# Kernel tuning notes

Hardware: AMD Instinct MI355X
Metric: run time of the kernel (lower is better)

The kernel has to match this reference:

```python
import jax, jax.numpy as jnp
import numpy as np

NUM_HEADS = 16
HEAD_DIM = 64
MODEL_DIM = NUM_HEADS * HEAD_DIM  # 1024
N_TOKENS = 121
BATCH = 1024
DISTURB_HEADS = np.array([0, 3], dtype=int)


def setup_inputs() -> dict:
    key = jax.random.key(0)
    ks = jax.random.split(key, 8)
    scale = 1.0 / np.sqrt(MODEL_DIM)
    return {
        "query": jax.random.normal(ks[0], (BATCH, MODEL_DIM), dtype=jnp.float32),
        "key": jax.random.normal(ks[1], (BATCH, N_TOKENS, MODEL_DIM), dtype=jnp.float32),
        "value": jax.random.normal(ks[2], (BATCH, N_TOKENS, MODEL_DIM), dtype=jnp.float32),
        "Wq": jax.random.normal(ks[3], (MODEL_DIM, MODEL_DIM), dtype=jnp.float32) * scale,
        "bq": jnp.zeros((MODEL_DIM,), dtype=jnp.float32),
        "Wk": jax.random.normal(ks[4], (MODEL_DIM, MODEL_DIM), dtype=jnp.float32) * scale,
        "bk": jnp.zeros((MODEL_DIM,), dtype=jnp.float32),
        "Wv": jax.random.normal(ks[5], (MODEL_DIM, MODEL_DIM), dtype=jnp.float32) * scale,
        "bv": jnp.zeros((MODEL_DIM,), dtype=jnp.float32),
    }


def reference(query, key, value, Wq, bq, Wk, bk, Wv, bv):
    B, N, _ = key.shape
    H, d = NUM_HEADS, HEAD_DIM
    # Linear projections (plain GEMMs)
    q_proj = query @ Wq + bq            # [B, H*d]
    k_proj = key @ Wk + bk              # [B, N, H*d]
    v_proj = value @ Wv + bv            # [B, N, H*d]

    q = q_proj.reshape(B, H, d)         # [B, H, d]
    k = k_proj.reshape(B, N, H, d)      # [B, N, H, d]
    v = v_proj.reshape(B, N, H, d)

    # single-query scores per head: [B, H, N]
    scores = jnp.einsum('bhd,bnhd->bhn', q, k)
    # head-wise disturb override: masked heads get all-ones scores
    mask = jnp.zeros((H,), dtype=bool).at[DISTURB_HEADS].set(True)[None, :, None]
    scores = jnp.where(mask, jnp.ones_like(scores), scores)
    # note: original scales by sqrt(d * H), not sqrt(d)
    scores = scores / jnp.sqrt(jnp.asarray(d * H, dtype=scores.dtype))
    weights = jax.nn.softmax(scores, axis=-1)   # [B, H, N]
    output = jnp.einsum('bhn,bnhd->bhd', weights, v).reshape(B, H * d)
    return (output, weights)
```

## Files before the change

### kernel.cpp

```cpp
#include <hip/hip_runtime.h>
#include <hip/hip_bf16.h>

#define NHEADS 16
#define HDIM   64
#define MDIM   1024
#define NTOK   121
#define NBATCH 1024

typedef __attribute__((ext_vector_type(4))) float f32x4;
typedef __attribute__((ext_vector_type(4))) short s16x4;
typedef __attribute__((ext_vector_type(8))) short s16x8;

#define WAIT_VM(n)  asm volatile("s_waitcnt vmcnt(" #n ")" ::: "memory")
#define WAIT_LGKM0() asm volatile("s_waitcnt lgkmcnt(0)" ::: "memory")

__device__ __forceinline__ short f2bf(float f) {
  __hip_bfloat16 h = __float2bfloat16(f);
  return __builtin_bit_cast(short, h);
}

#define GLDS(gptr, lptr)                                                        \
  __builtin_amdgcn_global_load_lds(                                             \
      (const __attribute__((address_space(1))) void*)(gptr),                    \
      (__attribute__((address_space(3))) void*)(lptr), 16, 0, 0)

__global__ __launch_bounds__(256) void kTransW(const float* __restrict__ Wq,
                                               const float* __restrict__ Wk,
                                               const float* __restrict__ Wv,
                                               short* __restrict__ Wt) {
  int bid = blockIdx.x;
  int m = bid >> 8, tile = bid & 255;
  int tr = tile >> 4, tc = tile & 15;
  const float* W = (m == 0) ? Wq : (m == 1) ? Wk : Wv;
  short* T = Wt + (size_t)m * (MDIM * MDIM);
  __shared__ float tl[64][68];
  int t = threadIdx.x;
  int c4 = t & 15, r0 = t >> 4;
#pragma unroll
  for (int i = 0; i < 4; ++i) {
    int kr = r0 + i * 16;
    f32x4 v = *(const f32x4*)(W + (size_t)(tr * 64 + kr) * MDIM + tc * 64 + c4 * 4);
    *(f32x4*)&tl[kr][c4 * 4] = v;
  }
  __syncthreads();
#pragma unroll
  for (int i = 0; i < 4; ++i) {
    int n = r0 + i * 16;
    s16x4 o;
    o.x = f2bf(tl[c4 * 4 + 0][n]);
    o.y = f2bf(tl[c4 * 4 + 1][n]);
    o.z = f2bf(tl[c4 * 4 + 2][n]);
    o.w = f2bf(tl[c4 * 4 + 3][n]);
    *(s16x4*)(T + (size_t)(tc * 64 + n) * MDIM + tr * 64 + c4 * 4) = o;
  }
}

__device__ __forceinline__ void gemm_core(const float* __restrict__ A, int mrows,
                                          const short* __restrict__ Wt, int c0,
                                          short* Alds, short* Bl0, short* Bl1,
                                          f32x4 acc[4][4], int t) {
  int wid = t >> 6, lane = t & 63;
  int wr = wid >> 1, wc = wid & 1;
  int li = lane & 15, lg = lane >> 4;
  int kq = t & 15, r0s = t >> 4;
#pragma unroll
  for (int fm = 0; fm < 4; ++fm)
#pragma unroll
    for (int fn = 0; fn < 4; ++fn) acc[fm][fn] = (f32x4)0.0f;

  int rhi[4];
#pragma unroll
  for (int i = 0; i < 4; ++i) {
    int row = r0s + 64 + (i << 4);
    rhi[i] = row < mrows ? row : mrows - 1;
  }
#pragma unroll
  for (int i = 0; i < 4; ++i) {
    int cl = wid * 32 + i * 8 + (lane >> 3);
    int jg = (lane & 7) ^ (cl & 7);
    GLDS(Wt + (size_t)(c0 + cl) * MDIM + jg * 8, Bl0 + (wid * 32 + i * 8) * 64);
  }
  f32x4 rLo[4];
#pragma unroll
  for (int i = 0; i < 4; ++i)
    rLo[i] = *(const f32x4*)(A + (size_t)(r0s + (i << 4)) * MDIM + kq * 4);

  for (int kt = 0; kt < 16; ++kt) {
    int k0 = kt * 64;
    short* Bcur = (kt & 1) ? Bl1 : Bl0;
    short* Bnxt = (kt & 1) ? Bl0 : Bl1;
    int kn = (kt < 15) ? k0 + 64 : 0;

    f32x4 rHi[4];
#pragma unroll
    for (int i = 0; i < 4; ++i)
      rHi[i] = *(const f32x4*)(A + (size_t)rhi[i] * MDIM + k0 + kq * 4);

    WAIT_VM(4);
    __builtin_amdgcn_s_barrier();
#pragma unroll
    for (int i = 0; i < 4; ++i) {
      int row = r0s + (i << 4);
      s16x4 b4;
      b4.x = f2bf(rLo[i].x); b4.y = f2bf(rLo[i].y);
      b4.z = f2bf(rLo[i].z); b4.w = f2bf(rLo[i].w);
      int byte = (row * 128 + kq * 8) ^ ((row & 7) << 4);
      *(s16x4*)((char*)Alds + byte) = b4;
    }
#pragma unroll
    for (int i = 0; i < 4; ++i) {
      int cl = wid * 32 + i * 8 + (lane >> 3);
      int jg = (lane & 7) ^ (cl & 7);
      GLDS(Wt + (size_t)(c0 + cl) * MDIM + kn + jg * 8, Bnxt + (wid * 32 + i * 8) * 64);
    }
    WAIT_VM(4);
#pragma unroll
    for (int i = 0; i < 4; ++i) {
      int row = r0s + 64 + (i << 4);
      s16x4 b4;
      b4.x = f2bf(rHi[i].x); b4.y = f2bf(rHi[i].y);
      b4.z = f2bf(rHi[i].z); b4.w = f2bf(rHi[i].w);
      int byte = (row * 128 + kq * 8) ^ ((row & 7) << 4);
      *(s16x4*)((char*)Alds + byte) = b4;
    }
#pragma unroll
    for (int i = 0; i < 4; ++i)
      rLo[i] = *(const f32x4*)(A + (size_t)(r0s + (i << 4)) * MDIM + kn + kq * 4);

    WAIT_LGKM0();
    __builtin_amdgcn_s_barrier();
#pragma unroll
    for (int ks = 0; ks < 2; ++ks) {
      s16x8 af[4];
      int kb = ks * 64 + lg * 16;
#pragma unroll
      for (int fm = 0; fm < 4; ++fm) {
        int row = wr * 64 + fm * 16 + li;
        int byte = (row * 128 + kb) ^ ((row & 7) << 4);
        af[fm] = *(s16x8*)((char*)Alds + byte);
      }
#pragma unroll
      for (int fn = 0; fn < 4; ++fn) {
        int col = wc * 64 + fn * 16 + li;
        int byte = (col * 128 + kb) ^ ((col & 7) << 4);
        s16x8 bfv = *(s16x8*)((char*)Bcur + byte);
#pragma unroll
        for (int fm = 0; fm < 4; ++fm)
          acc[fm][fn] = __builtin_amdgcn_mfma_f32_16x16x32_bf16(af[fm], bfv,
                                                                acc[fm][fn], 0, 0, 0);
      }
    }
  }
}

__global__ __launch_bounds__(256, 3) void kQProj(const float* __restrict__ query,
                                                 const short* __restrict__ WtQ,
                                                 const float* __restrict__ bq,
                                                 float* __restrict__ qp) {
  __shared__ alignas(16) short Alds[128 * 64];
  __shared__ alignas(16) short Bl0[128 * 64];
  __shared__ alignas(16) short Bl1[128 * 64];
  int bid = blockIdx.x;
  int rt = bid >> 3, ct = bid & 7;
  f32x4 acc[4][4];
  int t = threadIdx.x;
  gemm_core(query + (size_t)rt * 128 * MDIM, 128, WtQ, ct * 128, Alds, Bl0, Bl1, acc, t);
  int wid = t >> 6, lane = t & 63;
  int wr = wid >> 1, wc = wid & 1, li = lane & 15, lg = lane >> 4;
#pragma unroll
  for (int fn = 0; fn < 4; ++fn) {
    int col = ct * 128 + wc * 64 + fn * 16 + li;
    float bqv = bq[col];
#pragma unroll
    for (int fm = 0; fm < 4; ++fm)
#pragma unroll
      for (int rr = 0; rr < 4; ++rr) {
        int row = rt * 128 + wr * 64 + fm * 16 + lg * 4 + rr;
        qp[(size_t)row * MDIM + col] = acc[fm][fn][rr] + bqv;
      }
  }
}

__global__ __launch_bounds__(256, 3) void kG(const float* __restrict__ qp,
                                             const short* __restrict__ WtK,
                                             short* __restrict__ g) {
  __shared__ alignas(16) short Alds[128 * 64];
  __shared__ alignas(16) short Blds[128 * 64];
  int bid = blockIdx.x;
  int h = bid >> 6, bt = (bid >> 3) & 7, it = bid & 7;
  int t = threadIdx.x;
  int wid = t >> 6, lane = t & 63;
  int wr = wid >> 1, wc = wid & 1, li = lane & 15, lg = lane >> 4;
  int kq = t & 15, r0s = t >> 4;
#pragma unroll
  for (int i = 0; i < 8; ++i) {
    int r = r0s + 16 * i;
    f32x4 v = *(const f32x4*)(qp + (size_t)(bt * 128 + r) * MDIM + h * 64 + kq * 4);
    s16x4 b4;
    b4.x = f2bf(v.x); b4.y = f2bf(v.y); b4.z = f2bf(v.z); b4.w = f2bf(v.w);
    int byte = (r * 128 + kq * 8) ^ ((r & 7) << 4);
    *(s16x4*)((char*)Alds + byte) = b4;
  }
  {
    int jr = t >> 2, qc = t & 3;
#pragma unroll
    for (int q = 0; q < 4; ++q) {
      s16x8 v = *(const s16x8*)(WtK + (size_t)(h * 64 + jr) * MDIM + it * 128 +
                                qc * 32 + q * 8);
#pragma unroll
      for (int e = 0; e < 8; ++e) {
        int i = qc * 32 + q * 8 + e;
        int byte = (i * 128 + jr * 2) ^ ((i & 7) << 4);
        *(short*)((char*)Blds + byte) = v[e];
      }
    }
  }
  __syncthreads();
  f32x4 acc[4][4];
#pragma unroll
  for (int fm = 0; fm < 4; ++fm)
#pragma unroll
    for (int fn = 0; fn < 4; ++fn) acc[fm][fn] = (f32x4)0.0f;
#pragma unroll
  for (int ks = 0; ks < 2; ++ks) {
    int kb = ks * 64 + lg * 16;
    s16x8 af[4];
#pragma unroll
    for (int fm = 0; fm < 4; ++fm) {
      int row = wr * 64 + fm * 16 + li;
      int byte = (row * 128 + kb) ^ ((row & 7) << 4);
      af[fm] = *(s16x8*)((char*)Alds + byte);
    }
#pragma unroll
    for (int fn = 0; fn < 4; ++fn) {
      int col = wc * 64 + fn * 16 + li;
      int byte = (col * 128 + kb) ^ ((col & 7) << 4);
      s16x8 bfv = *(s16x8*)((char*)Blds + byte);
#pragma unroll
      for (int fm = 0; fm < 4; ++fm)
        acc[fm][fn] = __builtin_amdgcn_mfma_f32_16x16x32_bf16(af[fm], bfv,
                                                              acc[fm][fn], 0, 0, 0);
    }
  }
#pragma unroll
  for (int fm = 0; fm < 4; ++fm)
#pragma unroll
    for (int rr = 0; rr < 4; ++rr) {
      int b = bt * 128 + wr * 64 + fm * 16 + lg * 4 + rr;
      short* gp = g + ((size_t)b * 16 + h) * 1024 + it * 128;
#pragma unroll
      for (int fn = 0; fn < 4; ++fn)
        gp[wc * 64 + fn * 16 + li] = f2bf(acc[fm][fn][rr]);
    }
}

__global__ __launch_bounds__(512, 4) void kW(const float* __restrict__ key,
                                             const short* __restrict__ g,
                                             float* __restrict__ weights) {
  __shared__ alignas(16) short Klds[128 * 64];
  __shared__ alignas(16) short Glds[16 * 1024];
  __shared__ float s_lds[16][132];
  int b = blockIdx.x;
  int t = threadIdx.x;
  int wid = t >> 6, lane = t & 63, li = lane & 15, lg = lane >> 4;
  int kq = t & 15, r0s = t >> 4;
  int rcl[4];
#pragma unroll
  for (int i = 0; i < 4; ++i) {
    int r = r0s + 32 * i;
    rcl[i] = r < NTOK ? r : NTOK - 1;
  }
  const float* A = key + (size_t)b * NTOK * MDIM;
  const short* gb = g + (size_t)b * 16384;
#pragma unroll
  for (int q = 0; q < 4; ++q) {
    int c = q * 512 + t;
    s16x8 v = *(const s16x8*)(gb + c * 8);
    int byte = ((c >> 7) * 2048 + (c & 127) * 16) ^ (((c >> 7) & 7) << 4);
    *(s16x8*)((char*)Glds + byte) = v;
  }
  f32x4 rA[4];
#pragma unroll
  for (int i = 0; i < 4; ++i)
    rA[i] = *(const f32x4*)(A + (size_t)rcl[i] * MDIM + kq * 4);
  f32x4 acc = (f32x4)0.0f;

  for (int kt = 0; kt < 16; ++kt) {
    int kn = (kt < 15) ? (kt + 1) * 64 : 0;
    WAIT_VM(0);
    __builtin_amdgcn_s_barrier();
#pragma unroll
    for (int i = 0; i < 4; ++i) {
      int row = r0s + 32 * i;
      s16x4 b4;
      b4.x = f2bf(rA[i].x); b4.y = f2bf(rA[i].y);
      b4.z = f2bf(rA[i].z); b4.w = f2bf(rA[i].w);
      int byte = (row * 128 + kq * 8) ^ ((row & 7) << 4);
      *(s16x4*)((char*)Klds + byte) = b4;
    }
#pragma unroll
    for (int i = 0; i < 4; ++i)
      rA[i] = *(const f32x4*)(A + (size_t)rcl[i] * MDIM + kn + kq * 4);
    WAIT_LGKM0();
    __builtin_amdgcn_s_barrier();
#pragma unroll
    for (int ks = 0; ks < 2; ++ks) {
      int kb = ks * 64 + lg * 16;
      int row = wid * 16 + li;
      s16x8 af = *(s16x8*)((char*)Klds + ((row * 128 + kb) ^ ((row & 7) << 4)));
      int kel = kt * 64 + ks * 32 + lg * 8;
      s16x8 bf = *(s16x8*)((char*)Glds + ((li * 2048 + kel * 2) ^ ((li & 7) << 4)));
      acc = __builtin_amdgcn_mfma_f32_16x16x32_bf16(af, bf, acc, 0, 0, 0);
    }
  }
#pragma unroll
  for (int rr = 0; rr < 4; ++rr) s_lds[li][wid * 16 + lg * 4 + rr] = acc[rr];
  __syncthreads();
#pragma unroll
  for (int hh = 0; hh < 2; ++hh) {
    int h = wid * 2 + hh;
    int n0 = lane, n1 = lane + 64;
    bool v0 = (n0 < NTOK), v1 = (n1 < NTOK);
    float w0, w1;
    if (h == 0 || h == 3) {
      w0 = 1.f / NTOK; w1 = 1.f / NTOK;
    } else {
      const float kinv = 1.f / 32.f;
      float s0 = v0 ? s_lds[h][n0] * kinv : -1e30f;
      float s1 = v1 ? s_lds[h][n1] * kinv : -1e30f;
      float m = fmaxf(s0, s1);
#pragma unroll
      for (int msk = 1; msk < 64; msk <<= 1) m = fmaxf(m, __shfl_xor(m, msk));
      float e0 = v0 ? __expf(s0 - m) : 0.f;
      float e1 = v1 ? __expf(s1 - m) : 0.f;
      float s = e0 + e1;
#pragma unroll
      for (int msk = 1; msk < 64; msk <<= 1) s += __shfl_xor(s, msk);
      float inv = 1.f / s;
      w0 = e0 * inv; w1 = e1 * inv;
    }
    float* wp = weights + ((size_t)b * NHEADS + h) * NTOK;
    if (v0) wp[n0] = w0;
    if (v1) wp[n1] = w1;
  }
}

__global__ __launch_bounds__(512, 4) void kV(const float* __restrict__ value,
                                             const float* __restrict__ weights,
                                             float* __restrict__ vbar) {
  __shared__ float w_lds[16][128];
  int b = blockIdx.x;
  int t = threadIdx.x;
  int grp = t >> 7, ic = t & 127;
#pragma unroll
  for (int q = 0; q < 4; ++q) {
    int idx = q * 512 + t;
    int h = idx >> 7, n = idx & 127;
    w_lds[h][n] = (n < NTOK) ? weights[((size_t)b * NHEADS + h) * NTOK + n] : 0.f;
  }
  __syncthreads();
  const float* V = value + (size_t)b * NTOK * MDIM;
  f32x4 a0[4], a1[4];
#pragma unroll
  for (int hh = 0; hh < 4; ++hh) { a0[hh] = (f32x4)0.0f; a1[hh] = (f32x4)0.0f; }
#pragma unroll 2
  for (int n = 0; n < NTOK; ++n) {
    f32x4 v0 = *(const f32x4*)(V + (size_t)n * MDIM + ic * 8);
    f32x4 v1 = *(const f32x4*)(V + (size_t)n * MDIM + ic * 8 + 4);
#pragma unroll
    for (int hh = 0; hh < 4; ++hh) {
      float wn = w_lds[grp * 4 + hh][n];
      a0[hh] += wn * v0;
      a1[hh] += wn * v1;
    }
  }
#pragma unroll
  for (int hh = 0; hh < 4; ++hh) {
    float* vp = vbar + ((size_t)b * 16 + grp * 4 + hh) * 1024 + ic * 8;
    *(f32x4*)vp = a0[hh];
    *(f32x4*)(vp + 4) = a1[hh];
  }
}

__global__ __launch_bounds__(256, 3) void kO(const float* __restrict__ vbar,
                                             const short* __restrict__ WtV,
                                             const float* __restrict__ bv,
                                             float* __restrict__ outp) {
  __shared__ alignas(16) short Alds[128 * 64];
  __shared__ alignas(16) short Blds[64 * 64];
  int bid = blockIdx.x;
  int bt = bid >> 4, h = bid & 15;
  int t = threadIdx.x;
  int wid = t >> 6, lane = t & 63;
  int wr = wid >> 1, wc = wid & 1, li = lane & 15, lg = lane >> 4;
  int kq = t & 15, r0s = t >> 4;
  const float* A = vbar + (size_t)bt * 128 * 16384 + (size_t)h * 1024;
  f32x4 acc[4][2];
#pragma unroll
  for (int fm = 0; fm < 4; ++fm)
#pragma unroll
    for (int fn = 0; fn < 2; ++fn) acc[fm][fn] = (f32x4)0.0f;
  f32x4 rLo[4];
#pragma unroll
  for (int i = 0; i < 4; ++i)
    rLo[i] = *(const f32x4*)(A + (size_t)(r0s + 16 * i) * 16384 + kq * 4);

  for (int kt = 0; kt < 16; ++kt) {
    int k0 = kt * 64;
    __syncthreads();
    f32x4 rHi[4];
#pragma unroll
    for (int i = 0; i < 4; ++i)
      rHi[i] = *(const f32x4*)(A + (size_t)(r0s + 64 + 16 * i) * 16384 + k0 + kq * 4);
#pragma unroll
    for (int j = 0; j < 2; ++j) {
      int cl = wid * 16 + j * 8 + (lane >> 3);
      int jg = (lane & 7) ^ (cl & 7);
      GLDS(WtV + (size_t)(h * 64 + cl) * MDIM + k0 + jg * 8,
           Blds + (wid * 16 + j * 8) * 64);
    }
#pragma unroll
    for (int i = 0; i < 4; ++i) {
      int row = r0s + 16 * i;
      s16x4 b4;
      b4.x = f2bf(rLo[i].x); b4.y = f2bf(rLo[i].y);
      b4.z = f2bf(rLo[i].z); b4.w = f2bf(rLo[i].w);
      int byte = (row * 128 + kq * 8) ^ ((row & 7) << 4);
      *(s16x4*)((char*)Alds + byte) = b4;
    }
#pragma unroll
    for (int i = 0; i < 4; ++i) {
      int row = r0s + 64 + 16 * i;
      s16x4 b4;
      b4.x = f2bf(rHi[i].x); b4.y = f2bf(rHi[i].y);
      b4.z = f2bf(rHi[i].z); b4.w = f2bf(rHi[i].w);
      int byte = (row * 128 + kq * 8) ^ ((row & 7) << 4);
      *(s16x4*)((char*)Alds + byte) = b4;
    }
    __syncthreads();
    {
      int k1 = (kt < 15) ? k0 + 64 : 0;
#pragma unroll
      for (int i = 0; i < 4; ++i)
        rLo[i] = *(const f32x4*)(A + (size_t)(r0s + 16 * i) * 16384 + k1 + kq * 4);
    }
#pragma unroll
    for (int ks = 0; ks < 2; ++ks) {
      int kb = ks * 64 + lg * 16;
      s16x8 af[4];
#pragma unroll
      for (int fm = 0; fm < 4; ++fm) {
        int row = wr * 64 + fm * 16 + li;
        int byte = (row * 128 + kb) ^ ((row & 7) << 4);
        af[fm] = *(s16x8*)((char*)Alds + byte);
      }
#pragma unroll
      for (int fn = 0; fn < 2; ++fn) {
        int col = wc * 32 + fn * 16 + li;
        int byte = (col * 128 + kb) ^ ((col & 7) << 4);
        s16x8 bfv = *(s16x8*)((char*)Blds + byte);
#pragma unroll
        for (int fm = 0; fm < 4; ++fm)
          acc[fm][fn] = __builtin_amdgcn_mfma_f32_16x16x32_bf16(af[fm], bfv,
                                                                acc[fm][fn], 0, 0, 0);
      }
    }
  }
#pragma unroll
  for (int fn = 0; fn < 2; ++fn) {
    int cg = h * 64 + wc * 32 + fn * 16 + li;
    float bvv = bv[cg];
#pragma unroll
    for (int fm = 0; fm < 4; ++fm)
#pragma unroll
      for (int rr = 0; rr < 4; ++rr) {
        int row = bt * 128 + wr * 64 + fm * 16 + lg * 4 + rr;
        outp[(size_t)row * MDIM + cg] = acc[fm][fn][rr] + bvv;
      }
  }
}

extern "C" void kernel_launch(void* const* d_in, const int* in_sizes, int n_in,
                              void* d_out, int out_size, void* d_ws, size_t ws_size,
                              hipStream_t stream) {
  const float* query = (const float*)d_in[0];
  const float* key   = (const float*)d_in[1];
  const float* value = (const float*)d_in[2];
  const float* Wq    = (const float*)d_in[3];
  const float* bq    = (const float*)d_in[4];
  const float* Wk    = (const float*)d_in[5];
  const float* bk    = (const float*)d_in[6];
  const float* Wv    = (const float*)d_in[7];
  const float* bv    = (const float*)d_in[8];
  (void)bk;

  float* out     = (float*)d_out;
  float* weights = out + (size_t)NBATCH * MDIM;

  char* ws = (char*)d_ws;
  short* Wt   = (short*)ws;
  float* qp   = (float*)(ws + 6u  * 1024 * 1024);
  short* g    = (short*)(ws + 10u * 1024 * 1024);
  float* vbar = (float*)(ws + 48u * 1024 * 1024);

  kTransW<<<dim3(768),  dim3(256), 0, stream>>>(Wq, Wk, Wv, Wt);
  kQProj <<<dim3(64),   dim3(256), 0, stream>>>(query, Wt, bq, qp);
  kG     <<<dim3(1024), dim3(256), 0, stream>>>(qp, Wt + (size_t)MDIM * MDIM, g);
  kW     <<<dim3(1024), dim3(512), 0, stream>>>(key, g, weights);
  kV     <<<dim3(1024), dim3(512), 0, stream>>>(value, weights, vbar);
  kO     <<<dim3(128),  dim3(256), 0, stream>>>(vbar, Wt + 2 * (size_t)MDIM * MDIM,
                                                bv, out);
}
```

Before: 379.2 us.

## Double-buffer key tiles in kW and store vbar as bf16 for direct LDS loads

After: 315.0 us. 16.9% less time.

```diff
diff --git a/kernel.cpp b/kernel.cpp
--- a/kernel.cpp
+++ b/kernel.cpp
@@ -254,10 +254,11 @@
     }
 }
 
-__global__ __launch_bounds__(512, 4) void kW(const float* __restrict__ key,
-                                             const short* __restrict__ g,
-                                             float* __restrict__ weights) {
-  __shared__ alignas(16) short Klds[128 * 64];
+__global__ __launch_bounds__(512) void kW(const float* __restrict__ key,
+                                          const short* __restrict__ g,
+                                          float* __restrict__ weights) {
+  __shared__ alignas(16) short Kl0[128 * 64];
+  __shared__ alignas(16) short Kl1[128 * 64];
   __shared__ alignas(16) short Glds[16 * 1024];
   __shared__ float s_lds[16][132];
   int b = blockIdx.x;
@@ -279,36 +280,69 @@
     int byte = ((c >> 7) * 2048 + (c & 127) * 16) ^ (((c >> 7) & 7) << 4);
     *(s16x8*)((char*)Glds + byte) = v;
   }
-  f32x4 rA[4];
+  f32x4 rA0[4], rA1[4];
 #pragma unroll
   for (int i = 0; i < 4; ++i)
-    rA[i] = *(const f32x4*)(A + (size_t)rcl[i] * MDIM + kq * 4);
+    rA0[i] = *(const f32x4*)(A + (size_t)rcl[i] * MDIM + kq * 4);
+#pragma unroll
+  for (int i = 0; i < 4; ++i)
+    rA1[i] = *(const f32x4*)(A + (size_t)rcl[i] * MDIM + 64 + kq * 4);
+  WAIT_LGKM0();
+  __builtin_amdgcn_s_barrier();
   f32x4 acc = (f32x4)0.0f;
 
-  for (int kt = 0; kt < 16; ++kt) {
-    int kn = (kt < 15) ? (kt + 1) * 64 : 0;
-    WAIT_VM(0);
-    __builtin_amdgcn_s_barrier();
+  for (int kt = 0; kt < 16; kt += 2) {
+    WAIT_VM(4);
 #pragma unroll
     for (int i = 0; i < 4; ++i) {
       int row = r0s + 32 * i;
       s16x4 b4;
-      b4.x = f2bf(rA[i].x); b4.y = f2bf(rA[i].y);
-      b4.z = f2bf(rA[i].z); b4.w = f2bf(rA[i].w);
+      b4.x = f2bf(rA0[i].x); b4.y = f2bf(rA0[i].y);
+      b4.z = f2bf(rA0[i].z); b4.w = f2bf(rA0[i].w);
       int byte = (row * 128 + kq * 8) ^ ((row & 7) << 4);
-      *(s16x4*)((char*)Klds + byte) = b4;
-    }
-#pragma unroll
-    for (int i = 0; i < 4; ++i)
-      rA[i] = *(const f32x4*)(A + (size_t)rcl[i] * MDIM + kn + kq * 4);
+      *(s16x4*)((char*)Kl0 + byte) = b4;
+    }
+    {
+      int kn = (kt + 2 < 16) ? (kt + 2) * 64 : 0;
+#pragma unroll
+      for (int i = 0; i < 4; ++i)
+        rA0[i] = *(const f32x4*)(A + (size_t)rcl[i] * MDIM + kn + kq * 4);
+    }
     WAIT_LGKM0();
     __builtin_amdgcn_s_barrier();
 #pragma unroll
     for (int ks = 0; ks < 2; ++ks) {
       int kb = ks * 64 + lg * 16;
       int row = wid * 16 + li;
-      s16x8 af = *(s16x8*)((char*)Klds + ((row * 128 + kb) ^ ((row & 7) << 4)));
+      s16x8 af = *(s16x8*)((char*)Kl0 + ((row * 128 + kb) ^ ((row & 7) << 4)));
       int kel = kt * 64 + ks * 32 + lg * 8;
+      s16x8 bf = *(s16x8*)((char*)Glds + ((li * 2048 + kel * 2) ^ ((li & 7) << 4)));
+      acc = __builtin_amdgcn_mfma_f32_16x16x32_bf16(af, bf, acc, 0, 0, 0);
+    }
+    WAIT_VM(4);
+#pragma unroll
+    for (int i = 0; i < 4; ++i) {
+      int row = r0s + 32 * i;
+      s16x4 b4;
+      b4.x = f2bf(rA1[i].x); b4.y = f2bf(rA1[i].y);
+      b4.z = f2bf(rA1[i].z); b4.w = f2bf(rA1[i].w);
+      int byte = (row * 128 + kq * 8) ^ ((row & 7) << 4);
+      *(s16x4*)((char*)Kl1 + byte) = b4;
+    }
+    {
+      int kn = (kt + 3 < 16) ? (kt + 3) * 64 : 64;
+#pragma unroll
+      for (int i = 0; i < 4; ++i)
+        rA1[i] = *(const f32x4*)(A + (size_t)rcl[i] * MDIM + kn + kq * 4);
+    }
+    WAIT_LGKM0();
+    __builtin_amdgcn_s_barrier();
+#pragma unroll
+    for (int ks = 0; ks < 2; ++ks) {
+      int kb = ks * 64 + lg * 16;
+      int row = wid * 16 + li;
+      s16x8 af = *(s16x8*)((char*)Kl1 + ((row * 128 + kb) ^ ((row & 7) << 4)));
+      int kel = (kt + 1) * 64 + ks * 32 + lg * 8;
       s16x8 bf = *(s16x8*)((char*)Glds + ((li * 2048 + kel * 2) ^ ((li & 7) << 4)));
       acc = __builtin_amdgcn_mfma_f32_16x16x32_bf16(af, bf, acc, 0, 0, 0);
     }
@@ -347,7 +381,7 @@
 
 __global__ __launch_bounds__(512, 4) void kV(const float* __restrict__ value,
                                              const float* __restrict__ weights,
-                                             float* __restrict__ vbar) {
+                                             short* __restrict__ vbar) {
   __shared__ float w_lds[16][128];
   int b = blockIdx.x;
   int t = threadIdx.x;
@@ -363,7 +397,7 @@
   f32x4 a0[4], a1[4];
 #pragma unroll
   for (int hh = 0; hh < 4; ++hh) { a0[hh] = (f32x4)0.0f; a1[hh] = (f32x4)0.0f; }
-#pragma unroll 2
+#pragma unroll 4
   for (int n = 0; n < NTOK; ++n) {
     f32x4 v0 = *(const f32x4*)(V + (size_t)n * MDIM + ic * 8);
     f32x4 v1 = *(const f32x4*)(V + (size_t)n * MDIM + ic * 8 + 4);
@@ -376,13 +410,16 @@
   }
 #pragma unroll
   for (int hh = 0; hh < 4; ++hh) {
-    float* vp = vbar + ((size_t)b * 16 + grp * 4 + hh) * 1024 + ic * 8;
-    *(f32x4*)vp = a0[hh];
-    *(f32x4*)(vp + 4) = a1[hh];
-  }
-}
-
-__global__ __launch_bounds__(256, 3) void kO(const float* __restrict__ vbar,
+    s16x8 o;
+    o[0] = f2bf(a0[hh].x); o[1] = f2bf(a0[hh].y);
+    o[2] = f2bf(a0[hh].z); o[3] = f2bf(a0[hh].w);
+    o[4] = f2bf(a1[hh].x); o[5] = f2bf(a1[hh].y);
+    o[6] = f2bf(a1[hh].z); o[7] = f2bf(a1[hh].w);
+    *(s16x8*)(vbar + ((size_t)b * 16 + grp * 4 + hh) * 1024 + ic * 8) = o;
+  }
+}
+
+__global__ __launch_bounds__(256, 3) void kO(const short* __restrict__ vbar,
                                              const short* __restrict__ WtV,
                                              const float* __restrict__ bv,
                                              float* __restrict__ outp) {
@@ -393,25 +430,22 @@
   int t = threadIdx.x;
   int wid = t >> 6, lane = t & 63;
   int wr = wid >> 1, wc = wid & 1, li = lane & 15, lg = lane >> 4;
-  int kq = t & 15, r0s = t >> 4;
-  const float* A = vbar + (size_t)bt * 128 * 16384 + (size_t)h * 1024;
   f32x4 acc[4][2];
 #pragma unroll
   for (int fm = 0; fm < 4; ++fm)
 #pragma unroll
     for (int fn = 0; fn < 2; ++fn) acc[fm][fn] = (f32x4)0.0f;
-  f32x4 rLo[4];
-#pragma unroll
-  for (int i = 0; i < 4; ++i)
-    rLo[i] = *(const f32x4*)(A + (size_t)(r0s + 16 * i) * 16384 + kq * 4);
 
   for (int kt = 0; kt < 16; ++kt) {
     int k0 = kt * 64;
     __syncthreads();
-    f32x4 rHi[4];
-#pragma unroll
-    for (int i = 0; i < 4; ++i)
-      rHi[i] = *(const f32x4*)(A + (size_t)(r0s + 64 + 16 * i) * 16384 + k0 + kq * 4);
+#pragma unroll
+    for (int i = 0; i < 4; ++i) {
+      int lrow = wid * 32 + i * 8 + (lane >> 3);
+      int jg = (lane & 7) ^ (lrow & 7);
+      GLDS(vbar + ((size_t)(bt * 128 + lrow) * 16 + h) * 1024 + k0 + jg * 8,
+           Alds + (wid * 32 + i * 8) * 64);
+    }
 #pragma unroll
     for (int j = 0; j < 2; ++j) {
       int cl = wid * 16 + j * 8 + (lane >> 3);
@@ -419,31 +453,7 @@
       GLDS(WtV + (size_t)(h * 64 + cl) * MDIM + k0 + jg * 8,
            Blds + (wid * 16 + j * 8) * 64);
     }
-#pragma unroll
-    for (int i = 0; i < 4; ++i) {
-      int row = r0s + 16 * i;
-      s16x4 b4;
-      b4.x = f2bf(rLo[i].x); b4.y = f2bf(rLo[i].y);
-      b4.z = f2bf(rLo[i].z); b4.w = f2bf(rLo[i].w);
-      int byte = (row * 128 + kq * 8) ^ ((row & 7) << 4);
-      *(s16x4*)((char*)Alds + byte) = b4;
-    }
-#pragma unroll
-    for (int i = 0; i < 4; ++i) {
-      int row = r0s + 64 + 16 * i;
-      s16x4 b4;
-      b4.x = f2bf(rHi[i].x); b4.y = f2bf(rHi[i].y);
-      b4.z = f2bf(rHi[i].z); b4.w = f2bf(rHi[i].w);
-      int byte = (row * 128 + kq * 8) ^ ((row & 7) << 4);
-      *(s16x4*)((char*)Alds + byte) = b4;
-    }
     __syncthreads();
-    {
-      int k1 = (kt < 15) ? k0 + 64 : 0;
-#pragma unroll
-      for (int i = 0; i < 4; ++i)
-        rLo[i] = *(const f32x4*)(A + (size_t)(r0s + 16 * i) * 16384 + k1 + kq * 4);
-    }
 #pragma unroll
     for (int ks = 0; ks < 2; ++ks) {
       int kb = ks * 64 + lg * 16;
@@ -501,7 +511,7 @@
   short* Wt   = (short*)ws;
   float* qp   = (float*)(ws + 6u  * 1024 * 1024);
   short* g    = (short*)(ws + 10u * 1024 * 1024);
-  float* vbar = (float*)(ws + 48u * 1024 * 1024);
+  short* vbar = (short*)(ws + 48u * 1024 * 1024);
 
   kTransW<<<dim3(768),  dim3(256), 0, stream>>>(Wq, Wk, Wv, Wt);
   kQProj <<<dim3(64),   dim3(256), 0, stream>>>(query, Wt, bq, qp);
```
